# Performance work log

Hardware: AMD Instinct MI355X
Metric: run time of the kernel (lower is better)

Reference implementation:

```python
import math
import jax, jax.numpy as jnp
import numpy as np

B, M, N = 32, 64, 5000   # batch, multi_width (POMO rollouts), n_nodes
L, H, D, E = 100, 8, 16, 128  # local_size, head_num, qkv_dim, emb_dim


def setup_inputs() -> dict:
    key = jax.random.key(0)
    ks = jax.random.split(key, 10)
    return {
        "dist": jax.random.uniform(ks[0], (B, M, N), jnp.float32),
        "theta": jax.random.uniform(ks[1], (B, M, N), jnp.float32, minval=-math.pi, maxval=math.pi),
        "ninf_mask": jnp.zeros((B, M, N), jnp.float32),
        "W_init": jax.random.normal(ks[2], (E, 2), jnp.float32) * 0.1,
        "b_init": jax.random.normal(ks[3], (E,), jnp.float32) * 0.1,
        "cur_token": jax.random.uniform(ks[4], (E,), jnp.float32, minval=-1.0, maxval=1.0),
        "Wq": jax.random.normal(ks[5], (H * D, E), jnp.float32) * 0.05,
        "Wk": jax.random.normal(ks[6], (H * D, E), jnp.float32) * 0.05,
        "Wv": jax.random.normal(ks[7], (H * D, E), jnp.float32) * 0.05,
        "Wc": jax.random.normal(ks[8], (E, H * D), jnp.float32) * 0.05,
        "bc": jax.random.normal(ks[9], (E,), jnp.float32) * 0.05,
    }


def _positional_signal():
    # transformer sinusoidal encoding over the L gathered neighbors (E even -> no pad)
    num_ts = E // 2
    log_inc = math.log(10000.0) / max(num_ts - 1, 1)
    inv_ts = jnp.exp(jnp.arange(num_ts, dtype=jnp.float32) * -log_inc)
    pos = jnp.arange(L, dtype=jnp.float32)
    scaled = pos[:, None] * inv_ts[None, :]            # [L, E/2]
    return jnp.concatenate([jnp.sin(scaled), jnp.cos(scaled)], axis=1)  # [L, E]


def reference(dist, theta, ninf_mask, W_init, b_init, cur_token, Wq, Wk, Wv, Wc, bc):
    # mask out infeasible nodes (dist - (-inf) = +inf pushes them out of top-k)
    d = dist - ninf_mask                               # [B, M, N]
    neg_vals, idx = jax.lax.top_k(-d, L)               # smallest-L distances
    sorted_dist = -neg_vals                            # [B, M, L] ascending
    sorted_mask = jnp.take_along_axis(ninf_mask, idx, axis=-1)
    norm = sorted_dist.max(axis=-1, keepdims=True) + 1e-6
    sorted_dist = sorted_dist / norm
    sorted_theta = jnp.take_along_axis(theta, idx, axis=-1)
    sdt = jnp.stack([sorted_dist, sorted_theta], axis=-1)   # [B, M, L, 2]

    init_k = sdt @ W_init.T + b_init + _positional_signal()  # [B, M, L, E]

    # current-token query is a single shared learned vector -> q is [H, D]
    q = (Wq @ cur_token).reshape(H, D)
    kh = (init_k @ Wk.T).reshape(B, M, L, H, D)
    vh = (init_k @ Wv.T).reshape(B, M, L, H, D)

    score = jnp.einsum('hd,bmlhd->bhml', q, kh) / jnp.sqrt(jnp.float32(D))
    score = score + sorted_mask[:, None, :, :]              # rank3 ninf mask
    w = jax.nn.softmax(score, axis=-1)                      # [B, H, M, L]
    att = jnp.einsum('bhml,bmlhd->bmhd', w, vh).reshape(B, M, H * D)
    mh = att @ Wc.T + bc                                    # [B, M, E]

    score2 = jnp.einsum('bme,bmle->bml', mh, init_k) / jnp.sqrt(jnp.float32(E))

    # scatter local scores back into full [B, M, N]
    bi = jnp.arange(B)[:, None, None]
    mi = jnp.arange(M)[None, :, None]
    out = jnp.zeros((B, M, N), jnp.float32).at[bi, mi, idx].set(score2)
    return out
```

## Files before the change

### kernel.cpp

```cpp
#include <hip/hip_runtime.h>
#include <math.h>

#define B_ 32
#define M_ 64
#define N_ 5000
#define L_ 100
#define H_ 8
#define D_ 16
#define E_ 128
#define NI4 1250
#define NROW (B_ * M_)
#define NT 256
#define T0 0.033f
#define CAP 256

#define OFF_POSQ  0
#define OFF_C0    800
#define OFF_C1    808
#define OFF_C2    816
#define OFF_PV0   824
#define OFF_PV1   952
#define OFF_PVB   1080
#define OFF_WC0   1208
#define OFF_WC1   1336
#define OFF_WCB   1464
#define OFF_SB    1592
#define OFF_PCB   1596
#define OFF_PV    1696
#define OFF_PCT   14496

__device__ __forceinline__ unsigned int umap(float v) {
  unsigned int b = __float_as_uint(v);
  return (b & 0x80000000u) ? ~b : (b | 0x80000000u);
}
__device__ __forceinline__ float unmap(unsigned int u) {
  unsigned int b = (u & 0x80000000u) ? (u ^ 0x80000000u) : ~u;
  return __uint_as_float(b);
}

__global__ __launch_bounds__(128) void precomp(
    const float* __restrict__ Wq, const float* __restrict__ Wk,
    const float* __restrict__ cur, const float* __restrict__ Wi,
    const float* __restrict__ bi, const float* __restrict__ Wv,
    const float* __restrict__ Wc, const float* __restrict__ bc,
    float* __restrict__ ws)
{
  const int tid = threadIdx.x;
  const int blk = blockIdx.x;
  __shared__ float pr[E_];
  __shared__ float red[8];
  const int lane = tid & 63, wvv = tid >> 6;

  if (blk == 0) {
    float qsv = 0.f;
    for (int e = 0; e < E_; ++e) qsv = fmaf(Wq[tid * E_ + e], cur[e], qsv);
    float wk0=0,wk1=0,wkb=0,pv0=0,pv1=0,pvb=0,wc0=0,wc1=0,wcb=0;
    for (int e = 0; e < E_; ++e) {
      float wi0 = Wi[2*e], wi1 = Wi[2*e+1], bie = bi[e];
      float wk = Wk[tid*E_+e], wvx = Wv[tid*E_+e], wcc = Wc[e*(H_*D_)+tid];
      wk0=fmaf(wk,wi0,wk0);  wk1=fmaf(wk,wi1,wk1);  wkb=fmaf(wk,bie,wkb);
      pv0=fmaf(wvx,wi0,pv0); pv1=fmaf(wvx,wi1,pv1); pvb=fmaf(wvx,bie,pvb);
      wc0=fmaf(wcc,wi0,wc0); wc1=fmaf(wcc,wi1,wc1); wcb=fmaf(wcc,bie,wcb);
    }
    ws[OFF_PV0+tid]=pv0; ws[OFF_PV1+tid]=pv1; ws[OFF_PVB+tid]=pvb;
    ws[OFF_WC0+tid]=wc0; ws[OFF_WC1+tid]=wc1; ws[OFF_WCB+tid]=wcb;
    float c0 = qsv*wk0, c1 = qsv*wk1, c2 = qsv*wkb;
    for (int off = 1; off < 16; off <<= 1) {
      c0 += __shfl_xor(c0, off, 16); c1 += __shfl_xor(c1, off, 16); c2 += __shfl_xor(c2, off, 16);
    }
    if ((tid & 15) == 0) {
      int h = tid >> 4;
      ws[OFF_C0+h] = c0*0.25f; ws[OFF_C1+h] = c1*0.25f; ws[OFF_C2+h] = c2*0.25f;
    }
    float p0 = Wi[2*tid]*bc[tid], p1 = Wi[2*tid+1]*bc[tid], p2 = bi[tid]*bc[tid];
    for (int off = 32; off > 0; off >>= 1) {
      p0 += __shfl_xor(p0, off, 64); p1 += __shfl_xor(p1, off, 64); p2 += __shfl_xor(p2, off, 64);
    }
    if (lane == 0) { red[wvv*3+0]=p0; red[wvv*3+1]=p1; red[wvv*3+2]=p2; }
    __syncthreads();
    if (tid == 0) {
      ws[OFF_SB+0]=red[0]+red[3]; ws[OFF_SB+1]=red[1]+red[4]; ws[OFF_SB+2]=red[2]+red[5];
    }
  } else {
    const int l = blk - 1;
    const float log_inc = 0.14619588050755848f;
    {
      int j = tid & 63;
      float scaled = (float)l * expf(-(float)j * log_inc);
      pr[tid] = (tid < 64) ? sinf(scaled) : cosf(scaled);
    }
    __syncthreads();
    float qsv=0.f, pwk=0.f, accv=0.f, accc=0.f;
    for (int e = 0; e < E_; ++e) qsv = fmaf(Wq[tid*E_+e], cur[e], qsv);
    for (int e = 0; e < E_; ++e) {
      float p = pr[e];
      pwk  = fmaf(Wk[tid*E_+e], p, pwk);
      accv = fmaf(Wv[tid*E_+e], p, accv);
      accc = fmaf(Wc[e*(H_*D_)+tid], p, accc);
    }
    ws[OFF_PV  + l*(H_*D_) + tid] = accv;
    ws[OFF_PCT + tid*L_ + l] = accc;
    float pq = qsv * pwk;
    for (int off = 1; off < 16; off <<= 1) pq += __shfl_xor(pq, off, 16);
    if ((tid & 15) == 0) ws[OFF_POSQ + (tid>>4)*L_ + l] = pq * 0.25f;
    float pb = pr[tid] * bc[tid];
    for (int off = 32; off > 0; off >>= 1) pb += __shfl_xor(pb, off, 64);
    if (lane == 0) red[wvv] = pb;
    __syncthreads();
    if (tid == 0) ws[OFF_PCB + l] = red[0] + red[1];
  }
}

__global__ __launch_bounds__(NT) void row_kernel(
    const float* __restrict__ dist, const float* __restrict__ theta,
    const float* __restrict__ ninf, const float* __restrict__ ws,
    float* __restrict__ out)
{
  __shared__ unsigned long long sel[CAP];
  __shared__ unsigned int hist[256];
  __shared__ float sdv[128], stv[128], smv[128];
  __shared__ unsigned int idxs[128];
  __shared__ float att[H_ * D_];
  __shared__ unsigned int bitmap[160];
  __shared__ unsigned int hidx[256];
  __shared__ float hval[256];
  __shared__ unsigned int wsum[4];
  __shared__ unsigned int s_cnt, s_chosen, s_cumb2;
  __shared__ float s_nrm;

  const int tid = threadIdx.x;
  const int lane = tid & 63, wid = tid >> 6;
  const size_t base = (size_t)blockIdx.x * N_;
  const float4* d4 = (const float4*)(dist + base);
  const float4* n4 = (const float4*)(ninf + base);

  sel[tid] = ~0ull;
  if (tid == 0) s_cnt = 0u;

  unsigned int mask = 0u;
#pragma unroll
  for (int t = 0; t < 5; ++t) {
    int i4 = tid + NT * t;
    if (i4 < NI4) {
      float4 dv = d4[i4], nv = n4[i4];
      unsigned int m = ((dv.x - nv.x < T0) ? 1u : 0u)
                     | ((dv.y - nv.y < T0) ? 2u : 0u)
                     | ((dv.z - nv.z < T0) ? 4u : 0u)
                     | ((dv.w - nv.w < T0) ? 8u : 0u);
      mask |= m << (4 * t);
    }
  }
  __syncthreads();

  {
    unsigned int mk = mask;
    while (mk) {
      int b = __ffs(mk) - 1; mk &= mk - 1u;
      int t = b >> 2, c = b & 3;
      int i = 4 * (tid + NT * t) + c;
      float v = dist[base + i] - ninf[base + i];
      unsigned int p = atomicAdd(&s_cnt, 1u);
      if (p < CAP) sel[p] = ((unsigned long long)umap(v) << 13) | (unsigned)i;
    }
  }
  __syncthreads();
  const unsigned int cnt = s_cnt;

  if (cnt < (unsigned)L_ || cnt > (unsigned)CAP) {
    unsigned long long prefix = 0ull;
    unsigned int Krem = L_;
    for (int pass = 0; pass < 6; ++pass) {
      const int shift = 40 - 8 * pass;
      hist[tid] = 0u;
      __syncthreads();
      for (int t = 0; t < 5; ++t) {
        int i4 = tid + NT * t;
        if (i4 < NI4) {
          float4 dv = d4[i4], nv = n4[i4];
#pragma unroll
          for (int c = 0; c < 4; ++c) {
            float v = (&dv.x)[c] - (&nv.x)[c];
            unsigned long long key = ((unsigned long long)umap(v) << 13) | (unsigned)(4 * i4 + c);
            if ((key >> (shift + 8)) == prefix)
              atomicAdd(&hist[(unsigned)(key >> shift) & 0xFFu], 1u);
          }
        }
      }
      __syncthreads();
      unsigned int s = hist[tid];
      unsigned int v = s;
#pragma unroll
      for (int off = 1; off < 64; off <<= 1) {
        unsigned int x = __shfl_up(v, off, 64);
        if (lane >= off) v += x;
      }
      if (lane == 63) wsum[wid] = v;
      __syncthreads();
      { unsigned int add = 0; for (int ww = 0; ww < wid; ++ww) add += wsum[ww]; v += add; }
      unsigned int cb = v - s;
      if (cb < Krem && v >= Krem) { s_chosen = (unsigned)tid; s_cumb2 = cb; }
      __syncthreads();
      prefix = (prefix << 8) | s_chosen;
      Krem -= s_cumb2;
      __syncthreads();
    }
    const unsigned long long kpiv = prefix;
    sel[tid] = ~0ull;
    if (tid == 0) s_cnt = 0u;
    __syncthreads();
    for (int t = 0; t < 5; ++t) {
      int i4 = tid + NT * t;
      if (i4 < NI4) {
        float4 dv = d4[i4], nv = n4[i4];
#pragma unroll
        for (int c = 0; c < 4; ++c) {
          float v = (&dv.x)[c] - (&nv.x)[c];
          unsigned long long key = ((unsigned long long)umap(v) << 13) | (unsigned)(4 * i4 + c);
          if (key <= kpiv) {
            unsigned int p = atomicAdd(&s_cnt, 1u);
            if (p < CAP) sel[p] = key;
          }
        }
      }
    }
    __syncthreads();
  }

  {
    unsigned long long ka = sel[tid];
    const bool va = (ka != ~0ull);
    unsigned int ixa = (unsigned int)(ka & 0x1FFFull);
    float tha = 0.f, nma = 0.f;
    if (va) { tha = theta[base + ixa]; nma = ninf[base + ixa]; }
    int ra = 0;
#pragma unroll 8
    for (int j = 0; j < CAP; ++j) ra += (sel[j] < ka) ? 1 : 0;
    float sda = unmap((unsigned int)(ka >> 13));
    if (va && ra == L_ - 1) s_nrm = sda;
    __syncthreads();
    const float invn = 1.0f / (s_nrm + 1e-6f);
    if (va && ra < L_) { sdv[ra] = sda * invn; stv[ra] = tha; smv[ra] = nma; idxs[ra] = ixa; }
  }
  __syncthreads();

  if (tid < 128) {
    const int hh = tid >> 4, jj = tid & 15;
    float w7[7];
    float a0, a1;
    const float c0 = ws[OFF_C0 + hh], c1 = ws[OFF_C1 + hh], c2 = ws[OFF_C2 + hh];
    float mx = -INFINITY;
#pragma unroll
    for (int k = 0; k < 7; ++k) {
      int l = jj + 16 * k;
      float scv = -INFINITY;
      if (l < L_)
        scv = fmaf(sdv[l], c0, fmaf(stv[l], c1, c2 + ws[OFF_POSQ + hh * L_ + l] + smv[l]));
      w7[k] = scv;
      mx = fmaxf(mx, scv);
    }
#pragma unroll
    for (int off = 1; off <= 8; off <<= 1) mx = fmaxf(mx, __shfl_xor(mx, off, 64));
    float sum = 0.f;
#pragma unroll
    for (int k = 0; k < 7; ++k) { float e = expf(w7[k] - mx); w7[k] = e; sum += e; }
#pragma unroll
    for (int off = 1; off <= 8; off <<= 1) sum += __shfl_xor(sum, off, 64);
    const float inv = 1.0f / sum;
    a0 = 0.f; a1 = 0.f;
#pragma unroll
    for (int k = 0; k < 7; ++k) {
      int l = jj + 16 * k; int lc = (l < L_) ? l : 0;
      float wgt = w7[k] * inv; w7[k] = wgt;
      a0 = fmaf(wgt, sdv[lc], a0);
      a1 = fmaf(wgt, stv[lc], a1);
    }
#pragma unroll
    for (int off = 1; off <= 8; off <<= 1) { a0 += __shfl_xor(a0, off, 64); a1 += __shfl_xor(a1, off, 64); }
    {
      float part[16];
#pragma unroll
      for (int t = 0; t < 16; ++t) part[t] = 0.f;
#pragma unroll
      for (int k = 0; k < 7; ++k) {
        int l = jj + 16 * k;
        if (l < L_) {
          const float* pv = ws + OFF_PV + l * (H_ * D_) + hh * 16;
          float wgt = w7[k];
#pragma unroll
          for (int t = 0; t < 16; ++t) part[t] = fmaf(wgt, pv[t], part[t]);
        }
      }
#pragma unroll
      for (int off = 1; off <= 8; off <<= 1) {
#pragma unroll
        for (int t = 0; t < 16; ++t) part[t] += __shfl_xor(part[t], off, 64);
      }
#pragma unroll
      for (int t = 0; t < 16; ++t) {
        int hd = hh * 16 + t;
        att[hd] = fmaf(a0, ws[OFF_PV0 + hd], fmaf(a1, ws[OFF_PV1 + hd], ws[OFF_PVB + hd])) + part[t];
      }
    }
  } else {
    for (int j = tid - 128; j < 256; j += 128) hidx[j] = 0xFFFFFFFFu;
    for (int j = tid - 128; j < 160; j += 128) bitmap[j] = 0u;
  }
  __syncthreads();

  if (tid < 128) {
    float m0, m1, mb;
    {
      float x0 = att[lane], x1 = att[lane + 64];
      m0 = fmaf(x0, ws[OFF_WC0 + lane], x1 * ws[OFF_WC0 + lane + 64]);
      m1 = fmaf(x0, ws[OFF_WC1 + lane], x1 * ws[OFF_WC1 + lane + 64]);
      mb = fmaf(x0, ws[OFF_WCB + lane], x1 * ws[OFF_WCB + lane + 64]);
#pragma unroll
      for (int off = 1; off < 64; off <<= 1) {
        m0 += __shfl_xor(m0, off, 64);
        m1 += __shfl_xor(m1, off, 64);
        mb += __shfl_xor(mb, off, 64);
      }
      m0 += ws[OFF_SB + 0]; m1 += ws[OFF_SB + 1]; mb += ws[OFF_SB + 2];
    }
    if (tid < L_) {
      float acc = ws[OFF_PCB + tid];
#pragma unroll 16
      for (int hd = 0; hd < H_ * D_; ++hd) acc = fmaf(att[hd], ws[OFF_PCT + hd * L_ + tid], acc);
      const float SC = 0.08838834764831845f;
      float s2v = (fmaf(sdv[tid], m0, fmaf(stv[tid], m1, mb)) + acc) * SC;
      unsigned int idx = idxs[tid] & 0x1FFFu;
      unsigned int p = idx & 255u;
      for (int probe = 0; probe < 256; ++probe) {
        if (atomicCAS(&hidx[p], 0xFFFFFFFFu, idx) == 0xFFFFFFFFu) break;
        p = (p + 1) & 255u;
      }
      hval[p] = s2v;
      if (idx < (unsigned)N_) atomicOr(&bitmap[idx >> 5], 1u << (idx & 31));
    }
  }
  __syncthreads();

  float4* o4 = (float4*)(out + base);
#pragma unroll
  for (int t = 0; t < 5; ++t) {
    int i4 = tid + NT * t;
    if (i4 < NI4) {
      unsigned int wbits = (bitmap[i4 >> 3] >> ((i4 & 7) * 4)) & 0xFu;
      float4 o = make_float4(0.f, 0.f, 0.f, 0.f);
      if (wbits) {
#pragma unroll
        for (int c = 0; c < 4; ++c) {
          if ((wbits >> c) & 1u) {
            unsigned int idx = (unsigned int)(4 * i4 + c);
            unsigned int p = idx & 255u;
            float val = 0.f;
            for (int probe = 0; probe < 256; ++probe) {
              unsigned int h = hidx[p];
              if (h == idx) { val = hval[p]; break; }
              if (h == 0xFFFFFFFFu) break;
              p = (p + 1) & 255u;
            }
            (&o.x)[c] = val;
          }
        }
      }
      o4[i4] = o;
    }
  }
}

extern "C" void kernel_launch(void* const* d_in, const int* in_sizes, int n_in,
                              void* d_out, int out_size, void* d_ws, size_t ws_size,
                              hipStream_t stream) {
  const float* dist = (const float*)d_in[0];
  const float* theta = (const float*)d_in[1];
  const float* ninf = (const float*)d_in[2];
  const float* Wi   = (const float*)d_in[3];
  const float* bi   = (const float*)d_in[4];
  const float* cur  = (const float*)d_in[5];
  const float* Wq   = (const float*)d_in[6];
  const float* Wk   = (const float*)d_in[7];
  const float* Wv   = (const float*)d_in[8];
  const float* Wc   = (const float*)d_in[9];
  const float* bcv  = (const float*)d_in[10];
  float* out = (float*)d_out;
  float* ws  = (float*)d_ws;

  precomp<<<dim3(L_ + 1), dim3(128), 0, stream>>>(Wq, Wk, cur, Wi, bi, Wv, Wc, bcv, ws);
  row_kernel<<<dim3(NROW), dim3(NT), 0, stream>>>(dist, theta, ninf, ws, out);
}
```

Baseline: 77.38 us.

## Process two rows per block, prefetching second row into LDS asynchronously

Each block now handles two consecutive rows. The second row's dist and ninf arrays are streamed straight into LDS with global_load_lds while the first row is processed, so that row's load latency overlaps with compute. The block count is halved and about 40KB of LDS is added per block, which lowers occupancy. The fallback radix-select path still reads from global memory.

Result: slower. 99.96 us (+29.2%).

```diff
diff --git a/kernel.cpp b/kernel.cpp
--- a/kernel.cpp
+++ b/kernel.cpp
@@ -37,6 +37,11 @@
   unsigned int b = (u & 0x80000000u) ? (u ^ 0x80000000u) : ~u;
   return __uint_as_float(b);
 }
+__device__ __forceinline__ void gload_lds16(const void* g, void* l) {
+  __builtin_amdgcn_global_load_lds(
+      (const __attribute__((address_space(1))) void*)g,
+      (__attribute__((address_space(3))) void*)l, 16, 0, 0);
+}
 
 __global__ __launch_bounds__(128) void precomp(
     const float* __restrict__ Wq, const float* __restrict__ Wk,
@@ -116,6 +121,8 @@
     const float* __restrict__ ninf, const float* __restrict__ ws,
     float* __restrict__ out)
 {
+  __shared__ float ldsD[5120];
+  __shared__ float ldsN[5120];
   __shared__ unsigned long long sel[CAP];
   __shared__ unsigned int hist[256];
   __shared__ float sdv[128], stv[128], smv[128];
@@ -130,48 +137,123 @@
 
   const int tid = threadIdx.x;
   const int lane = tid & 63, wid = tid >> 6;
-  const size_t base = (size_t)blockIdx.x * N_;
-  const float4* d4 = (const float4*)(dist + base);
-  const float4* n4 = (const float4*)(ninf + base);
-
-  sel[tid] = ~0ull;
-  if (tid == 0) s_cnt = 0u;
-
-  unsigned int mask = 0u;
-#pragma unroll
-  for (int t = 0; t < 5; ++t) {
-    int i4 = tid + NT * t;
-    if (i4 < NI4) {
-      float4 dv = d4[i4], nv = n4[i4];
-      unsigned int m = ((dv.x - nv.x < T0) ? 1u : 0u)
-                     | ((dv.y - nv.y < T0) ? 2u : 0u)
-                     | ((dv.z - nv.z < T0) ? 4u : 0u)
-                     | ((dv.w - nv.w < T0) ? 8u : 0u);
-      mask |= m << (4 * t);
+  const int row0 = blockIdx.x * 2;
+
+  {
+    const char* gD = (const char*)(dist + (size_t)(row0 + 1) * N_);
+    const char* gN = (const char*)(ninf + (size_t)(row0 + 1) * N_);
+#pragma unroll
+    for (int k = 0; k < 5; ++k) {
+      int ch = wid * 5 + k;
+      int off = ch * 1024 + lane * 16;
+      if (off > 19984) off = 19984;
+      gload_lds16(gD + off, &ldsD[ch * 256]);
+      gload_lds16(gN + off, &ldsN[ch * 256]);
     }
   }
-  __syncthreads();
-
+
+  unsigned int mask0 = 0u;
   {
-    unsigned int mk = mask;
-    while (mk) {
-      int b = __ffs(mk) - 1; mk &= mk - 1u;
-      int t = b >> 2, c = b & 3;
-      int i = 4 * (tid + NT * t) + c;
-      float v = dist[base + i] - ninf[base + i];
-      unsigned int p = atomicAdd(&s_cnt, 1u);
-      if (p < CAP) sel[p] = ((unsigned long long)umap(v) << 13) | (unsigned)i;
+    const float4* d4 = (const float4*)(dist + (size_t)row0 * N_);
+    const float4* n4 = (const float4*)(ninf + (size_t)row0 * N_);
+#pragma unroll
+    for (int t = 0; t < 5; ++t) {
+      int i4 = tid + NT * t;
+      if (i4 < NI4) {
+        float4 dv = d4[i4], nv = n4[i4];
+        unsigned int m = ((dv.x - nv.x < T0) ? 1u : 0u)
+                       | ((dv.y - nv.y < T0) ? 2u : 0u)
+                       | ((dv.z - nv.z < T0) ? 4u : 0u)
+                       | ((dv.w - nv.w < T0) ? 8u : 0u);
+        mask0 |= m << (4 * t);
+      }
     }
   }
-  __syncthreads();
-  const unsigned int cnt = s_cnt;
-
-  if (cnt < (unsigned)L_ || cnt > (unsigned)CAP) {
-    unsigned long long prefix = 0ull;
-    unsigned int Krem = L_;
-    for (int pass = 0; pass < 6; ++pass) {
-      const int shift = 40 - 8 * pass;
-      hist[tid] = 0u;
+
+  for (int rr = 0; rr < 2; ++rr) {
+    const size_t base = (size_t)(row0 + rr) * N_;
+    const float4* d4 = (const float4*)(dist + base);
+    const float4* n4 = (const float4*)(ninf + base);
+
+    sel[tid] = ~0ull;
+    hidx[tid] = 0xFFFFFFFFu;
+    if (tid < 160) bitmap[tid] = 0u;
+    if (tid == 0) s_cnt = 0u;
+    __syncthreads();
+
+    if (rr == 0) {
+      unsigned int mk = mask0;
+      while (mk) {
+        int b = __ffs(mk) - 1; mk &= mk - 1u;
+        int t = b >> 2, c = b & 3;
+        int i = 4 * (tid + NT * t) + c;
+        float v = dist[base + i] - ninf[base + i];
+        unsigned int p = atomicAdd(&s_cnt, 1u);
+        if (p < CAP) sel[p] = ((unsigned long long)umap(v) << 13) | (unsigned)i;
+      }
+    } else {
+      const float4* lD = (const float4*)ldsD;
+      const float4* lN = (const float4*)ldsN;
+#pragma unroll
+      for (int t = 0; t < 5; ++t) {
+        int i4 = tid + NT * t;
+        if (i4 < NI4) {
+          float4 dv = lD[i4], nv = lN[i4];
+#pragma unroll
+          for (int c = 0; c < 4; ++c) {
+            float v = (&dv.x)[c] - (&nv.x)[c];
+            if (v < T0) {
+              unsigned int p = atomicAdd(&s_cnt, 1u);
+              if (p < CAP) sel[p] = ((unsigned long long)umap(v) << 13) | (unsigned)(4 * i4 + c);
+            }
+          }
+        }
+      }
+    }
+    __syncthreads();
+    const unsigned int cnt = s_cnt;
+
+    if (cnt < (unsigned)L_ || cnt > (unsigned)CAP) {
+      unsigned long long prefix = 0ull;
+      unsigned int Krem = L_;
+      for (int pass = 0; pass < 6; ++pass) {
+        const int shift = 40 - 8 * pass;
+        hist[tid] = 0u;
+        __syncthreads();
+        for (int t = 0; t < 5; ++t) {
+          int i4 = tid + NT * t;
+          if (i4 < NI4) {
+            float4 dv = d4[i4], nv = n4[i4];
+#pragma unroll
+            for (int c = 0; c < 4; ++c) {
+              float v = (&dv.x)[c] - (&nv.x)[c];
+              unsigned long long key = ((unsigned long long)umap(v) << 13) | (unsigned)(4 * i4 + c);
+              if ((key >> (shift + 8)) == prefix)
+                atomicAdd(&hist[(unsigned)(key >> shift) & 0xFFu], 1u);
+            }
+          }
+        }
+        __syncthreads();
+        unsigned int s = hist[tid];
+        unsigned int v = s;
+#pragma unroll
+        for (int off = 1; off < 64; off <<= 1) {
+          unsigned int x = __shfl_up(v, off, 64);
+          if (lane >= off) v += x;
+        }
+        if (lane == 63) wsum[wid] = v;
+        __syncthreads();
+        { unsigned int add = 0; for (int ww = 0; ww < wid; ++ww) add += wsum[ww]; v += add; }
+        unsigned int cb = v - s;
+        if (cb < Krem && v >= Krem) { s_chosen = (unsigned)tid; s_cumb2 = cb; }
+        __syncthreads();
+        prefix = (prefix << 8) | s_chosen;
+        Krem -= s_cumb2;
+        __syncthreads();
+      }
+      const unsigned long long kpiv = prefix;
+      sel[tid] = ~0ull;
+      if (tid == 0) s_cnt = 0u;
       __syncthreads();
       for (int t = 0; t < 5; ++t) {
         int i4 = tid + NT * t;
@@ -181,191 +263,157 @@
           for (int c = 0; c < 4; ++c) {
             float v = (&dv.x)[c] - (&nv.x)[c];
             unsigned long long key = ((unsigned long long)umap(v) << 13) | (unsigned)(4 * i4 + c);
-            if ((key >> (shift + 8)) == prefix)
-              atomicAdd(&hist[(unsigned)(key >> shift) & 0xFFu], 1u);
+            if (key <= kpiv) {
+              unsigned int p = atomicAdd(&s_cnt, 1u);
+              if (p < CAP) sel[p] = key;
+            }
           }
         }
       }
       __syncthreads();
-      unsigned int s = hist[tid];
-      unsigned int v = s;
-#pragma unroll
-      for (int off = 1; off < 64; off <<= 1) {
-        unsigned int x = __shfl_up(v, off, 64);
-        if (lane >= off) v += x;
-      }
-      if (lane == 63) wsum[wid] = v;
+    }
+
+    {
+      unsigned long long ka = sel[tid];
+      const bool va = (ka != ~0ull);
+      unsigned int ixa = (unsigned int)(ka & 0x1FFFull);
+      float tha = 0.f, nma = 0.f;
+      if (va) { tha = theta[base + ixa]; nma = ninf[base + ixa]; }
+      int ra = 0;
+#pragma unroll 8
+      for (int j = 0; j < CAP; ++j) ra += (sel[j] < ka) ? 1 : 0;
+      float sda = unmap((unsigned int)(ka >> 13));
+      if (va && ra == L_ - 1) s_nrm = sda;
       __syncthreads();
-      { unsigned int add = 0; for (int ww = 0; ww < wid; ++ww) add += wsum[ww]; v += add; }
-      unsigned int cb = v - s;
-      if (cb < Krem && v >= Krem) { s_chosen = (unsigned)tid; s_cumb2 = cb; }
-      __syncthreads();
-      prefix = (prefix << 8) | s_chosen;
-      Krem -= s_cumb2;
-      __syncthreads();
-    }
-    const unsigned long long kpiv = prefix;
-    sel[tid] = ~0ull;
-    if (tid == 0) s_cnt = 0u;
-    __syncthreads();
-    for (int t = 0; t < 5; ++t) {
-      int i4 = tid + NT * t;
-      if (i4 < NI4) {
-        float4 dv = d4[i4], nv = n4[i4];
-#pragma unroll
-        for (int c = 0; c < 4; ++c) {
-          float v = (&dv.x)[c] - (&nv.x)[c];
-          unsigned long long key = ((unsigned long long)umap(v) << 13) | (unsigned)(4 * i4 + c);
-          if (key <= kpiv) {
-            unsigned int p = atomicAdd(&s_cnt, 1u);
-            if (p < CAP) sel[p] = key;
-          }
-        }
-      }
-    }
-    __syncthreads();
-  }
-
-  {
-    unsigned long long ka = sel[tid];
-    const bool va = (ka != ~0ull);
-    unsigned int ixa = (unsigned int)(ka & 0x1FFFull);
-    float tha = 0.f, nma = 0.f;
-    if (va) { tha = theta[base + ixa]; nma = ninf[base + ixa]; }
-    int ra = 0;
-#pragma unroll 8
-    for (int j = 0; j < CAP; ++j) ra += (sel[j] < ka) ? 1 : 0;
-    float sda = unmap((unsigned int)(ka >> 13));
-    if (va && ra == L_ - 1) s_nrm = sda;
-    __syncthreads();
-    const float invn = 1.0f / (s_nrm + 1e-6f);
-    if (va && ra < L_) { sdv[ra] = sda * invn; stv[ra] = tha; smv[ra] = nma; idxs[ra] = ixa; }
-  }
-  __syncthreads();
-
-  if (tid < 128) {
-    const int hh = tid >> 4, jj = tid & 15;
-    float w7[7];
-    float a0, a1;
-    const float c0 = ws[OFF_C0 + hh], c1 = ws[OFF_C1 + hh], c2 = ws[OFF_C2 + hh];
-    float mx = -INFINITY;
-#pragma unroll
-    for (int k = 0; k < 7; ++k) {
-      int l = jj + 16 * k;
-      float scv = -INFINITY;
-      if (l < L_)
-        scv = fmaf(sdv[l], c0, fmaf(stv[l], c1, c2 + ws[OFF_POSQ + hh * L_ + l] + smv[l]));
-      w7[k] = scv;
-      mx = fmaxf(mx, scv);
-    }
-#pragma unroll
-    for (int off = 1; off <= 8; off <<= 1) mx = fmaxf(mx, __shfl_xor(mx, off, 64));
-    float sum = 0.f;
-#pragma unroll
-    for (int k = 0; k < 7; ++k) { float e = expf(w7[k] - mx); w7[k] = e; sum += e; }
-#pragma unroll
-    for (int off = 1; off <= 8; off <<= 1) sum += __shfl_xor(sum, off, 64);
-    const float inv = 1.0f / sum;
-    a0 = 0.f; a1 = 0.f;
-#pragma unroll
-    for (int k = 0; k < 7; ++k) {
-      int l = jj + 16 * k; int lc = (l < L_) ? l : 0;
-      float wgt = w7[k] * inv; w7[k] = wgt;
-      a0 = fmaf(wgt, sdv[lc], a0);
-      a1 = fmaf(wgt, stv[lc], a1);
-    }
-#pragma unroll
-    for (int off = 1; off <= 8; off <<= 1) { a0 += __shfl_xor(a0, off, 64); a1 += __shfl_xor(a1, off, 64); }
-    {
-      float part[16];
-#pragma unroll
-      for (int t = 0; t < 16; ++t) part[t] = 0.f;
+      const float invn = 1.0f / (s_nrm + 1e-6f);
+      if (va && ra < L_) { sdv[ra] = sda * invn; stv[ra] = tha; smv[ra] = nma; idxs[ra] = ixa; }
+    }
+    __syncthreads();
+
+    if (tid < 128) {
+      const int hh = tid >> 4, jj = tid & 15;
+      float w7[7];
+      float a0, a1;
+      const float c0 = ws[OFF_C0 + hh], c1 = ws[OFF_C1 + hh], c2 = ws[OFF_C2 + hh];
+      float mx = -INFINITY;
 #pragma unroll
       for (int k = 0; k < 7; ++k) {
         int l = jj + 16 * k;
-        if (l < L_) {
-          const float* pv = ws + OFF_PV + l * (H_ * D_) + hh * 16;
-          float wgt = w7[k];
-#pragma unroll
-          for (int t = 0; t < 16; ++t) part[t] = fmaf(wgt, pv[t], part[t]);
-        }
-      }
-#pragma unroll
-      for (int off = 1; off <= 8; off <<= 1) {
-#pragma unroll
-        for (int t = 0; t < 16; ++t) part[t] += __shfl_xor(part[t], off, 64);
-      }
-#pragma unroll
-      for (int t = 0; t < 16; ++t) {
-        int hd = hh * 16 + t;
-        att[hd] = fmaf(a0, ws[OFF_PV0 + hd], fmaf(a1, ws[OFF_PV1 + hd], ws[OFF_PVB + hd])) + part[t];
-      }
-    }
-  } else {
-    for (int j = tid - 128; j < 256; j += 128) hidx[j] = 0xFFFFFFFFu;
-    for (int j = tid - 128; j < 160; j += 128) bitmap[j] = 0u;
-  }
-  __syncthreads();
-
-  if (tid < 128) {
-    float m0, m1, mb;
+        float scv = -INFINITY;
+        if (l < L_)
+          scv = fmaf(sdv[l], c0, fmaf(stv[l], c1, c2 + ws[OFF_POSQ + hh * L_ + l] + smv[l]));
+        w7[k] = scv;
+        mx = fmaxf(mx, scv);
+      }
+#pragma unroll
+      for (int off = 1; off <= 8; off <<= 1) mx = fmaxf(mx, __shfl_xor(mx, off, 64));
+      float sum = 0.f;
+#pragma unroll
+      for (int k = 0; k < 7; ++k) { float e = expf(w7[k] - mx); w7[k] = e; sum += e; }
+#pragma unroll
+      for (int off = 1; off <= 8; off <<= 1) sum += __shfl_xor(sum, off, 64);
+      const float inv = 1.0f / sum;
+      a0 = 0.f; a1 = 0.f;
+#pragma unroll
+      for (int k = 0; k < 7; ++k) {
+        int l = jj + 16 * k; int lc = (l < L_) ? l : 0;
+        float wgt = w7[k] * inv; w7[k] = wgt;
+        a0 = fmaf(wgt, sdv[lc], a0);
+        a1 = fmaf(wgt, stv[lc], a1);
+      }
+#pragma unroll
+      for (int off = 1; off <= 8; off <<= 1) { a0 += __shfl_xor(a0, off, 64); a1 += __shfl_xor(a1, off, 64); }
+      {
+        float part[16];
+#pragma unroll
+        for (int t = 0; t < 16; ++t) part[t] = 0.f;
+#pragma unroll
+        for (int k = 0; k < 7; ++k) {
+          int l = jj + 16 * k;
+          if (l < L_) {
+            const float* pv = ws + OFF_PV + l * (H_ * D_) + hh * 16;
+            float wgt = w7[k];
+#pragma unroll
+            for (int t = 0; t < 16; ++t) part[t] = fmaf(wgt, pv[t], part[t]);
+          }
+        }
+#pragma unroll
+        for (int off = 1; off <= 8; off <<= 1) {
+#pragma unroll
+          for (int t = 0; t < 16; ++t) part[t] += __shfl_xor(part[t], off, 64);
+        }
+#pragma unroll
+        for (int t = 0; t < 16; ++t) {
+          int hd = hh * 16 + t;
+          att[hd] = fmaf(a0, ws[OFF_PV0 + hd], fmaf(a1, ws[OFF_PV1 + hd], ws[OFF_PVB + hd])) + part[t];
+        }
+      }
+    }
+    __syncthreads();
+
+    if (tid < 128) {
+      float m0, m1, mb;
+      {
+        float x0 = att[lane], x1 = att[lane + 64];
+        m0 = fmaf(x0, ws[OFF_WC0 + lane], x1 * ws[OFF_WC0 + lane + 64]);
+        m1 = fmaf(x0, ws[OFF_WC1 + lane], x1 * ws[OFF_WC1 + lane + 64]);
+        mb = fmaf(x0, ws[OFF_WCB + lane], x1 * ws[OFF_WCB + lane + 64]);
+#pragma unroll
+        for (int off = 1; off < 64; off <<= 1) {
+          m0 += __shfl_xor(m0, off, 64);
+          m1 += __shfl_xor(m1, off, 64);
+          mb += __shfl_xor(mb, off, 64);
+        }
+        m0 += ws[OFF_SB + 0]; m1 += ws[OFF_SB + 1]; mb += ws[OFF_SB + 2];
+      }
+      if (tid < L_) {
+        float acc = ws[OFF_PCB + tid];
+#pragma unroll 16
+        for (int hd = 0; hd < H_ * D_; ++hd) acc = fmaf(att[hd], ws[OFF_PCT + hd * L_ + tid], acc);
+        const float SC = 0.08838834764831845f;
+        float s2v = (fmaf(sdv[tid], m0, fmaf(stv[tid], m1, mb)) + acc) * SC;
+        unsigned int idx = idxs[tid] & 0x1FFFu;
+        unsigned int p = idx & 255u;
+        for (int probe = 0; probe < 256; ++probe) {
+          if (atomicCAS(&hidx[p], 0xFFFFFFFFu, idx) == 0xFFFFFFFFu) break;
+          p = (p + 1) & 255u;
+        }
+        hval[p] = s2v;
+        if (idx < (unsigned)N_) atomicOr(&bitmap[idx >> 5], 1u << (idx & 31));
+      }
+    }
+    __syncthreads();
+
     {
-      float x0 = att[lane], x1 = att[lane + 64];
-      m0 = fmaf(x0, ws[OFF_WC0 + lane], x1 * ws[OFF_WC0 + lane + 64]);
-      m1 = fmaf(x0, ws[OFF_WC1 + lane], x1 * ws[OFF_WC1 + lane + 64]);
-      mb = fmaf(x0, ws[OFF_WCB + lane], x1 * ws[OFF_WCB + lane + 64]);
-#pragma unroll
-      for (int off = 1; off < 64; off <<= 1) {
-        m0 += __shfl_xor(m0, off, 64);
-        m1 += __shfl_xor(m1, off, 64);
-        mb += __shfl_xor(mb, off, 64);
-      }
-      m0 += ws[OFF_SB + 0]; m1 += ws[OFF_SB + 1]; mb += ws[OFF_SB + 2];
-    }
-    if (tid < L_) {
-      float acc = ws[OFF_PCB + tid];
-#pragma unroll 16
-      for (int hd = 0; hd < H_ * D_; ++hd) acc = fmaf(att[hd], ws[OFF_PCT + hd * L_ + tid], acc);
-      const float SC = 0.08838834764831845f;
-      float s2v = (fmaf(sdv[tid], m0, fmaf(stv[tid], m1, mb)) + acc) * SC;
-      unsigned int idx = idxs[tid] & 0x1FFFu;
-      unsigned int p = idx & 255u;
-      for (int probe = 0; probe < 256; ++probe) {
-        if (atomicCAS(&hidx[p], 0xFFFFFFFFu, idx) == 0xFFFFFFFFu) break;
-        p = (p + 1) & 255u;
-      }
-      hval[p] = s2v;
-      if (idx < (unsigned)N_) atomicOr(&bitmap[idx >> 5], 1u << (idx & 31));
-    }
-  }
-  __syncthreads();
-
-  float4* o4 = (float4*)(out + base);
-#pragma unroll
-  for (int t = 0; t < 5; ++t) {
-    int i4 = tid + NT * t;
-    if (i4 < NI4) {
-      unsigned int wbits = (bitmap[i4 >> 3] >> ((i4 & 7) * 4)) & 0xFu;
-      float4 o = make_float4(0.f, 0.f, 0.f, 0.f);
-      if (wbits) {
-#pragma unroll
-        for (int c = 0; c < 4; ++c) {
-          if ((wbits >> c) & 1u) {
-            unsigned int idx = (unsigned int)(4 * i4 + c);
-            unsigned int p = idx & 255u;
-            float val = 0.f;
-            for (int probe = 0; probe < 256; ++probe) {
-              unsigned int h = hidx[p];
-              if (h == idx) { val = hval[p]; break; }
-              if (h == 0xFFFFFFFFu) break;
-              p = (p + 1) & 255u;
+      float4* o4 = (float4*)(out + base);
+#pragma unroll
+      for (int t = 0; t < 5; ++t) {
+        int i4 = tid + NT * t;
+        if (i4 < NI4) {
+          unsigned int wbits = (bitmap[i4 >> 3] >> ((i4 & 7) * 4)) & 0xFu;
+          float4 o = make_float4(0.f, 0.f, 0.f, 0.f);
+          if (wbits) {
+#pragma unroll
+            for (int c = 0; c < 4; ++c) {
+              if ((wbits >> c) & 1u) {
+                unsigned int idx = (unsigned int)(4 * i4 + c);
+                unsigned int p = idx & 255u;
+                float val = 0.f;
+                for (int probe = 0; probe < 256; ++probe) {
+                  unsigned int h = hidx[p];
+                  if (h == idx) { val = hval[p]; break; }
+                  if (h == 0xFFFFFFFFu) break;
+                  p = (p + 1) & 255u;
+                }
+                (&o.x)[c] = val;
+              }
             }
-            (&o.x)[c] = val;
           }
-        }
-      }
-      o4[i4] = o;
-    }
+          o4[i4] = o;
+        }
+      }
+    }
+    __syncthreads();
   }
 }
 
@@ -387,5 +435,5 @@
   float* ws  = (float*)d_ws;
 
   precomp<<<dim3(L_ + 1), dim3(128), 0, stream>>>(Wq, Wk, cur, Wi, bi, Wv, Wc, bcv, ws);
-  row_kernel<<<dim3(NROW), dim3(NT), 0, stream>>>(dist, theta, ninf, ws, out);
-}
+  row_kernel<<<dim3(NROW / 2), dim3(NT), 0, stream>>>(dist, theta, ninf, ws, out);
+}
```
